# Kernel optimization log

Hardware: AMD Instinct MI355X
Metric: run time of the kernel (lower is better)

The kernel has to match this reference:

```python
import jax, jax.numpy as jnp
import numpy as np

N, E, G = 50000, 320000, 256
BN_EPS = 1e-5
HEADS = 4


def _bn(x, g, b):
    # eval-mode BatchNorm1d with running_mean=0, running_var=1
    return g * (x * np.float32(1.0 / np.sqrt(1.0 + BN_EPS))) + b


def _mlp(x, w1, b1, w2, b2):
    return jax.nn.relu(x @ w1 + b1) @ w2 + b2


def _gatv2(x, src, dst, ea, lw, lb, rw, rb, ew, att, bias):
    n = x.shape[0]
    H = HEADS
    C = lw.shape[1] // H
    # self-loops with edge_attr = mean of incoming edge features (fill_value='mean')
    deg = jax.ops.segment_sum(jnp.ones((ea.shape[0],), x.dtype), dst, num_segments=n)
    loop_ea = jax.ops.segment_sum(ea, dst, num_segments=n) / jnp.maximum(deg, 1.0)[:, None]
    ar = jnp.arange(n)
    s = jnp.concatenate([src, ar])
    d = jnp.concatenate([dst, ar])
    ea_all = jnp.concatenate([ea, loop_ea], axis=0)
    xl = (x @ lw + lb).reshape(n, H, C)   # lin_l (source / message features)
    xr = (x @ rw + rb).reshape(n, H, C)   # lin_r (target)
    ee = (ea_all @ ew).reshape(-1, H, C)  # lin_edge (no bias)
    m = jax.nn.leaky_relu(xl[s] + xr[d] + ee, 0.2)       # [E+N, H, C]
    a = jnp.einsum('ehc,hc->eh', m, att)                 # attention logits
    amax = jax.ops.segment_max(a, d, num_segments=n)
    ex = jnp.exp(a - amax[d])
    den = jax.ops.segment_sum(ex, d, num_segments=n)
    w = ex / den[d]                                      # scatter-softmax over target
    out = jax.ops.segment_sum(xl[s] * w[..., None], d, num_segments=n)
    return out.reshape(n, H * C) + bias


def _meta(x, ea, u, src, dst, batch, ep, gp, up):
    # EdgeModel -> NodeModel(GATv2 + relu) -> GlobalModel (residuals=False, eval dropout)
    ea2 = _mlp(jnp.concatenate([x[src], x[dst], ea], axis=1), *ep)
    xn = jax.nn.relu(_gatv2(x, src, dst, ea2, *gp))
    pooled = jax.ops.segment_sum(xn, batch, num_segments=G)
    u2 = _mlp(jnp.concatenate([u, pooled], axis=1), *up)
    return xn, ea2, u2


def _forward(x, edge_attr, e1_w1, e1_b1, e1_w2, e1_b2, g1_lw, g1_lb, g1_rw, g1_rb, g1_ew, g1_att, g1_bias, u1_w1, u1_b1, u1_w2, u1_b2, bn_n_g, bn_n_b, bn_e_g, bn_e_b, bn_u_g, bn_u_b, e2_w1, e2_b1, e2_w2, e2_b2, g2_lw, g2_lb, g2_rw, g2_rb, g2_ew, g2_att, g2_bias, u2_w1, u2_b1, u2_w2, u2_b2, fc1_w, fc1_b, fc2_w, fc2_b, src, dst, batch):
    u0 = jnp.zeros((G, 256), x.dtype)
    x1, ea1, u1 = _meta(x, edge_attr, u0, src, dst, batch,
                        (e1_w1, e1_b1, e1_w2, e1_b2),
                        (g1_lw, g1_lb, g1_rw, g1_rb, g1_ew, g1_att, g1_bias),
                        (u1_w1, u1_b1, u1_w2, u1_b2))
    x1 = _bn(x1, bn_n_g, bn_n_b)
    ea1 = _bn(ea1, bn_e_g, bn_e_b)
    u1 = _bn(u1, bn_u_g, bn_u_b)
    _, _, u2 = _meta(x1, ea1, u1, src, dst, batch,
                     (e2_w1, e2_b1, e2_w2, e2_b2),
                     (g2_lw, g2_lb, g2_rw, g2_rb, g2_ew, g2_att, g2_bias),
                     (u2_w1, u2_b1, u2_w2, u2_b2))
    h = jax.nn.relu(u2 @ fc1_w + fc1_b)
    return h @ fc2_w + fc2_b


def setup_inputs() -> dict:
    key = jax.random.key(0)
    ks = iter(jax.random.split(key, 64))
    rp = lambda shape: jax.random.normal(next(ks), shape, jnp.float32) * 0.05
    inp = {}
    inp['x'] = jax.random.normal(next(ks), (N, 64), jnp.float32)
    inp['edge_attr'] = jax.random.normal(next(ks), (E, 16), jnp.float32)
    # layer 1: EdgeModel(64,16,h=64,out=128), GATv2(64->256,H=4,edge=128), Global(256+256->256)
    inp.update(e1_w1=rp((144, 64)), e1_b1=rp((64,)), e1_w2=rp((64, 128)), e1_b2=rp((128,)))
    inp.update(g1_lw=rp((64, 256)), g1_lb=rp((256,)), g1_rw=rp((64, 256)), g1_rb=rp((256,)),
               g1_ew=rp((128, 256)), g1_att=rp((4, 64)), g1_bias=rp((256,)))
    inp.update(u1_w1=rp((512, 256)), u1_b1=rp((256,)), u1_w2=rp((256, 256)), u1_b2=rp((256,)))
    inp.update(bn_n_g=jnp.ones((256,), jnp.float32), bn_n_b=jnp.zeros((256,), jnp.float32),
               bn_e_g=jnp.ones((128,), jnp.float32), bn_e_b=jnp.zeros((128,), jnp.float32),
               bn_u_g=jnp.ones((256,), jnp.float32), bn_u_b=jnp.zeros((256,), jnp.float32))
    # layer 2: EdgeModel(256,128,h=128,out=128), GATv2(256->256,H=4,edge=128), Global
    inp.update(e2_w1=rp((640, 128)), e2_b1=rp((128,)), e2_w2=rp((128, 128)), e2_b2=rp((128,)))
    inp.update(g2_lw=rp((256, 256)), g2_lb=rp((256,)), g2_rw=rp((256, 256)), g2_rb=rp((256,)),
               g2_ew=rp((128, 256)), g2_att=rp((4, 64)), g2_bias=rp((256,)))
    inp.update(u2_w1=rp((512, 256)), u2_b1=rp((256,)), u2_w2=rp((256, 256)), u2_b2=rp((256,)))
    inp.update(fc1_w=rp((256, 64)), fc1_b=rp((64,)), fc2_w=rp((64, 1)), fc2_b=rp((1,)))
    inp['edge_index'] = jax.random.randint(next(ks), (2, E), 0, N, jnp.int64)
    inp['batch'] = jnp.sort(jax.random.randint(next(ks), (N,), 0, G, jnp.int64))
    return inp


def reference(x, edge_attr, e1_w1, e1_b1, e1_w2, e1_b2, g1_lw, g1_lb, g1_rw, g1_rb, g1_ew, g1_att, g1_bias, u1_w1, u1_b1, u1_w2, u1_b2, bn_n_g, bn_n_b, bn_e_g, bn_e_b, bn_u_g, bn_u_b, e2_w1, e2_b1, e2_w2, e2_b2, g2_lw, g2_lb, g2_rw, g2_rb, g2_ew, g2_att, g2_bias, u2_w1, u2_b1, u2_w2, u2_b2, fc1_w, fc1_b, fc2_w, fc2_b, edge_index, batch):
    return _forward(x, edge_attr, e1_w1, e1_b1, e1_w2, e1_b2, g1_lw, g1_lb, g1_rw, g1_rb, g1_ew, g1_att, g1_bias, u1_w1, u1_b1, u1_w2, u1_b2, bn_n_g, bn_n_b, bn_e_g, bn_e_b, bn_u_g, bn_u_b, e2_w1, e2_b1, e2_w2, e2_b2, g2_lw, g2_lb, g2_rw, g2_rb, g2_ew, g2_att, g2_bias, u2_w1, u2_b1, u2_w2, u2_b2, fc1_w, fc1_b, fc2_w, fc2_b, edge_index[0], edge_index[1], batch)
```

## Files before the change

kernel.cpp:

```cpp
#include <hip/hip_runtime.h>
#include <hip/hip_bf16.h>
#include <hip/hip_fp8.h>
#include <cstdint>
#include <cstddef>

#define INVS 0.99999500003749968f
#define G_GRAPHS 256

using bf16 = __hip_bfloat16;
using short8 = __attribute__((ext_vector_type(8))) short;
using floatx4 = __attribute__((ext_vector_type(4))) float;

__device__ __forceinline__ unsigned short f2bf(float v) {
    union { float f; unsigned u; } x; x.f = v;
    unsigned r = x.u + 0x7fffu + ((x.u >> 16) & 1u);
    return (unsigned short)(r >> 16);
}
__device__ __forceinline__ float bfu(unsigned short u) { return __uint_as_float((unsigned)u << 16); }
__device__ __forceinline__ unsigned char f2fp8(float v) {
    __hip_fp8_e4m3 q(v); return q.__x;
}
__device__ __forceinline__ float fp82f(unsigned char b) {
    __hip_fp8_e4m3 q; q.__x = b; return (float)q;
}

__global__ void degi_k(const int* __restrict__ dst, int* __restrict__ degi, int E) {
    int gid = blockIdx.x * 256 + threadIdx.x;
    if (gid < E) atomicAdd(&degi[dst[gid]], 1);
}

__global__ __launch_bounds__(1024) void scan_blk_k(const int* __restrict__ degi,
                                                   int* __restrict__ off,
                                                   int* __restrict__ bsum, int N) {
    __shared__ int buf[1024];
    int t = threadIdx.x;
    int base = blockIdx.x * 2048;
    int i0 = base + 2 * t, i1 = base + 2 * t + 1;
    int v0 = (i0 < N) ? (degi[i0] + 1) : 0;
    int v1 = (i1 < N) ? (degi[i1] + 1) : 0;
    int s = v0 + v1;
    buf[t] = s;
    __syncthreads();
    for (int ofs = 1; ofs < 1024; ofs <<= 1) {
        int add = (t >= ofs) ? buf[t - ofs] : 0;
        __syncthreads();
        buf[t] += add;
        __syncthreads();
    }
    int excl = buf[t] - s;
    if (i0 < N) off[i0] = excl;
    if (i1 < N) off[i1] = excl + v0;
    if (t == 1023) bsum[blockIdx.x] = buf[1023];
}

__global__ void scan_top_k(const int* __restrict__ bsum, int* __restrict__ boff,
                           int* __restrict__ off, int NBLK, int N) {
    if (threadIdx.x == 0 && blockIdx.x == 0) {
        int run = 0;
        for (int i = 0; i < NBLK; ++i) { boff[i] = run; run += bsum[i]; }
        off[N] = run;
    }
}

__global__ void scan_add_k(int* __restrict__ off, const int* __restrict__ boff, int N) {
    int gid = blockIdx.x * 256 + threadIdx.x;
    if (gid < N) off[gid] += boff[gid >> 11];
}

__global__ void fill_csr_k(const int* __restrict__ src, const int* __restrict__ dst,
                           const int* __restrict__ off, int* __restrict__ fillc,
                           int* __restrict__ csr_src, int* __restrict__ csr_dst,
                           int* __restrict__ csr_eid, int* __restrict__ slot_of,
                           int E, int N) {
    int gid = blockIdx.x * 256 + threadIdx.x;
    if (gid < E) {
        int d = dst[gid];
        int slot = off[d] + atomicAdd(&fillc[d], 1);
        csr_src[slot] = src[gid];
        csr_dst[slot] = d;
        csr_eid[slot] = gid;
        slot_of[gid] = slot;
    }
    if (gid < N) {
        int slot = off[gid + 1] - 1;
        csr_src[slot] = gid;
        csr_dst[slot] = gid;
        csr_eid[slot] = E + gid;
    }
}

__global__ void conv_weights1_k(const float* __restrict__ w1, const float* __restrict__ w2,
                                short* __restrict__ w1s, short* __restrict__ w2s) {
    int gid = blockIdx.x * 256 + threadIdx.x;
    if (gid < 1280) {
        int f = gid >> 6, lane = gid & 63;
        int kk = f >> 2, tt = f & 3;
        int n = tt * 16 + (lane & 15);
        int k0 = kk * 32 + (lane >> 4) * 8;
        short8 v;
        for (int j = 0; j < 8; ++j) {
            int k = k0 + j;
            v[j] = (k < 144) ? (short)f2bf(w1[k * 64 + n]) : (short)0;
        }
        *(short8*)(w1s + (long long)gid * 8) = v;
    } else if (gid < 2304) {
        int g2 = gid - 1280;
        int f = g2 >> 6, lane = g2 & 63;
        int kk = f >> 3, tt = f & 7;
        int n = tt * 16 + (lane & 15);
        int k0 = kk * 32 + (lane >> 4) * 8;
        short8 v;
        for (int j = 0; j < 8; ++j) v[j] = (short)f2bf(w2[(k0 + j) * 128 + n]);
        *(short8*)(w2s + (long long)g2 * 8) = v;
    }
}

__global__ void conv_ew_k(const float* __restrict__ ew, short* __restrict__ ews) {
    int gid = blockIdx.x * 256 + threadIdx.x;
    if (gid >= 4096) return;
    int f = gid >> 6, lane = gid & 63;
    int kk = f >> 4, tt = f & 15;
    int n = tt * 16 + (lane & 15);
    int k0 = kk * 32 + (lane >> 4) * 8;
    short8 v;
    for (int j = 0; j < 8; ++j) v[j] = (short)f2bf(ew[(k0 + j) * 256 + n]);
    *(short8*)(ews + (long long)gid * 8) = v;
}

template <int K>
__global__ void conv_nodew_k(const float* __restrict__ wl, const float* __restrict__ wr,
                             short* __restrict__ out) {
    int gid = blockIdx.x * 256 + threadIdx.x;
    if (gid >= (K / 32) * 32 * 64) return;
    int f = gid >> 6, lane = gid & 63;
    int kk = f >> 5, tt = f & 31;
    int n = tt * 16 + (lane & 15);
    int k0 = kk * 32 + (lane >> 4) * 8;
    short8 v;
    for (int j = 0; j < 8; ++j) {
        int k = k0 + j;
        float x = (n < 256) ? wl[k * 256 + n] : wr[k * 256 + (n - 256)];
        v[j] = (short)f2bf(x);
    }
    *(short8*)(out + (long long)gid * 8) = v;
}

__global__ void conv_pre2w_k(const float* __restrict__ w1, short* __restrict__ out) {
    int gid = blockIdx.x * 256 + threadIdx.x;
    if (gid >= 8 * 16 * 64) return;
    int f = gid >> 6, lane = gid & 63;
    int kk = f >> 4, tt = f & 15;
    int n = tt * 16 + (lane & 15);
    int k0 = kk * 32 + (lane >> 4) * 8;
    short8 v;
    for (int j = 0; j < 8; ++j) {
        int k = k0 + j;
        float x = (n < 128) ? w1[k * 128 + n] : w1[(256 + k) * 128 + (n - 128)];
        v[j] = (short)f2bf(x);
    }
    *(short8*)(out + (long long)gid * 8) = v;
}

__global__ __launch_bounds__(256) void edge_mlp1_mfma_k(
    const float* __restrict__ x, const float* __restrict__ ea,
    const int* __restrict__ src, const int* __restrict__ dst,
    const int* __restrict__ slot_of,
    const short* __restrict__ w1s, const float* __restrict__ b1,
    const short* __restrict__ w2s, const float* __restrict__ b2,
    bf16* __restrict__ out, int E) {
    __shared__ short At[32][168];
    __shared__ short Ht[32][72];
    __shared__ int sdv[32][2];
    __shared__ int slt[32];
    int t = threadIdx.x;
    long long e0 = (long long)blockIdx.x * 32;
    if (t < 64) {
        int r = t & 31;
        long long e = e0 + r;
        int v = 0;
        if (e < E) v = (t < 32) ? src[e] : dst[e];
        sdv[r][t >> 5] = v;
    } else if (t < 96) {
        int r = t - 64;
        long long e = e0 + r;
        slt[r] = (e < E) ? slot_of[e] : -1;
    }
    __syncthreads();
    for (int i = t; i < 32 * 40; i += 256) {
        int r = i / 40, c = i - r * 40;
        long long e = e0 + r;
        float4 v = {0.f, 0.f, 0.f, 0.f};
        if (e < E) {
            if (c < 16)      v = *(const float4*)(x + (long long)sdv[r][0] * 64 + c * 4);
            else if (c < 32) v = *(const float4*)(x + (long long)sdv[r][1] * 64 + (c - 16) * 4);
            else if (c < 36) v = *(const float4*)(ea + e * 16 + (c - 32) * 4);
        }
        ushort4 pk;
        pk.x = f2bf(v.x); pk.y = f2bf(v.y); pk.z = f2bf(v.z); pk.w = f2bf(v.w);
        *(ushort4*)&At[r][c * 4] = pk;
    }
    __syncthreads();

    int w = t >> 6, lane = t & 63;
    int m0 = (w & 1) * 16;
    int lr = lane & 15, lq = lane >> 4;

    int nq1 = (w >> 1) * 2;
    floatx4 acc[2];
    for (int i = 0; i < 2; ++i) acc[i] = (floatx4){0.f, 0.f, 0.f, 0.f};
    for (int kk = 0; kk < 5; ++kk) {
        short8 a = *(const short8*)&At[m0 + lr][kk * 32 + lq * 8];
        for (int tt = 0; tt < 2; ++tt) {
            short8 b = *(const short8*)(w1s + ((long long)((kk * 4 + nq1 + tt) * 64 + lane)) * 8);
            acc[tt] = __builtin_amdgcn_mfma_f32_16x16x32_bf16(a, b, acc[tt], 0, 0, 0);
        }
    }
    for (int tt = 0; tt < 2; ++tt) {
        int col = (nq1 + tt) * 16 + lr;
        float bv = b1[col];
        for (int r = 0; r < 4; ++r)
            Ht[m0 + lq * 4 + r][col] = (short)f2bf(fmaxf(acc[tt][r] + bv, 0.f));
    }
    __syncthreads();

    int nq2 = (w >> 1) * 4;
    floatx4 acc2[4];
    for (int i = 0; i < 4; ++i) acc2[i] = (floatx4){0.f, 0.f, 0.f, 0.f};
    for (int kk = 0; kk < 2; ++kk) {
        short8 a = *(const short8*)&Ht[m0 + lr][kk * 32 + lq * 8];
        for (int tt = 0; tt < 4; ++tt) {
            short8 b = *(const short8*)(w2s + ((long long)((kk * 8 + nq2 + tt) * 64 + lane)) * 8);
            acc2[tt] = __builtin_amdgcn_mfma_f32_16x16x32_bf16(a, b, acc2[tt], 0, 0, 0);
        }
    }
    for (int tt = 0; tt < 4; ++tt) {
        int col = (nq2 + tt) * 16 + lr;
        float bv = b2[col];
        for (int r = 0; r < 4; ++r)
            At[m0 + lq * 4 + r][col] = (short)f2bf(acc2[tt][r] + bv);
    }
    __syncthreads();
    for (int i = t; i < 512; i += 256) {
        int r = i >> 4, c = i & 15;
        int s = slt[r];
        if (s >= 0)
            *(short8*)(void*)(out + (long long)s * 128 + c * 8) = *(const short8*)&At[r][c * 8];
    }
}

template <int K, typename T>
__global__ __launch_bounds__(256) void node_linear_mfma_k(
    const T* x, const short* __restrict__ ws,
    const float* __restrict__ bl, const float* __restrict__ br,
    bf16* __restrict__ xl, bf16* xr, int N) {
    __shared__ short At[16][K + 8];
    __shared__ short Ot[16][520];
    int t = threadIdx.x;
    long long n0 = (long long)blockIdx.x * 16;
    if (sizeof(T) == 4) {
        for (int i = t; i < 16 * (K / 4); i += 256) {
            int r = i / (K / 4), c = i % (K / 4);
            long long n = n0 + r;
            float4 v = {0.f, 0.f, 0.f, 0.f};
            if (n < N) v = *(const float4*)((const float*)x + n * K + c * 4);
            ushort4 pk;
            pk.x = f2bf(v.x); pk.y = f2bf(v.y); pk.z = f2bf(v.z); pk.w = f2bf(v.w);
            *(ushort4*)&At[r][c * 4] = pk;
        }
    } else {
        for (int i = t; i < 16 * (K / 8); i += 256) {
            int r = i / (K / 8), c = i % (K / 8);
            long long n = n0 + r;
            short8 v = {0, 0, 0, 0, 0, 0, 0, 0};
            if (n < N) v = *(const short8*)(const void*)((const bf16*)x + n * K + c * 8);
            *(short8*)&At[r][c * 8] = v;
        }
    }
    __syncthreads();

    int w = t >> 6, lane = t & 63;
    int nq = w * 8;
    int lr = lane & 15, lq = lane >> 4;

    floatx4 acc[8];
    for (int i = 0; i < 8; ++i) acc[i] = (floatx4){0.f, 0.f, 0.f, 0.f};
    for (int kk = 0; kk < K / 32; ++kk) {
        short8 a = *(const short8*)&At[lr][kk * 32 + lq * 8];
        for (int tt = 0; tt < 8; ++tt) {
            short8 b = *(const short8*)(ws + ((long long)((kk * 32 + nq + tt) * 64 + lane)) * 8);
            acc[tt] = __builtin_amdgcn_mfma_f32_16x16x32_bf16(a, b, acc[tt], 0, 0, 0);
        }
    }
    for (int tt = 0; tt < 8; ++tt) {
        int col = (nq + tt) * 16 + lr;
        float bv = (col < 256) ? bl[col] : br[col - 256];
        for (int r = 0; r < 4; ++r)
            Ot[lq * 4 + r][col] = (short)f2bf(acc[tt][r] + bv);
    }
    __syncthreads();
    for (int i = t; i < 1024; i += 256) {
        int r = i >> 6, c = i & 63;
        long long n = n0 + r;
        if (n < N) {
            short8 v = *(const short8*)&Ot[r][c * 8];
            if (c < 32) *(short8*)(void*)(xl + n * 256 + c * 8) = v;
            else        *(short8*)(void*)(xr + n * 256 + (c - 32) * 8) = v;
        }
    }
}

__global__ __launch_bounds__(256) void pre_mfma_k(
    const bf16* __restrict__ x, const short* __restrict__ ws,
    const float* __restrict__ bx, bf16* __restrict__ out, int N) {
    __shared__ short At[16][264];
    __shared__ short Ot[16][264];
    int t = threadIdx.x;
    long long n0 = (long long)blockIdx.x * 16;
    for (int i = t; i < 512; i += 256) {
        int r = i >> 5, c = i & 31;
        long long n = n0 + r;
        short8 v = {0, 0, 0, 0, 0, 0, 0, 0};
        if (n < N) v = *(const short8*)(const void*)(x + n * 256 + c * 8);
        *(short8*)&At[r][c * 8] = v;
    }
    __syncthreads();

    int w = t >> 6, lane = t & 63;
    int nq = w * 4;
    int lr = lane & 15, lq = lane >> 4;

    floatx4 acc[4];
    for (int i = 0; i < 4; ++i) acc[i] = (floatx4){0.f, 0.f, 0.f, 0.f};
    for (int kk = 0; kk < 8; ++kk) {
        short8 a = *(const short8*)&At[lr][kk * 32 + lq * 8];
        for (int tt = 0; tt < 4; ++tt) {
            short8 b = *(const short8*)(ws + ((long long)((kk * 16 + nq + tt) * 64 + lane)) * 8);
            acc[tt] = __builtin_amdgcn_mfma_f32_16x16x32_bf16(a, b, acc[tt], 0, 0, 0);
        }
    }
    for (int tt = 0; tt < 4; ++tt) {
        int col = (nq + tt) * 16 + lr;
        float bv = bx[col];
        for (int r = 0; r < 4; ++r)
            Ot[lq * 4 + r][col] = (short)f2bf(acc[tt][r] + bv);
    }
    __syncthreads();
    for (int i = t; i < 512; i += 256) {
        int r = i >> 5, c = i & 31;
        long long n = n0 + r;
        if (n < N)
            *(short8*)(void*)(out + n * 256 + c * 8) = *(const short8*)&Ot[r][c * 8];
    }
}

__global__ __launch_bounds__(256) void gemm_ee_k(
    const bf16* __restrict__ ea_slot, const short* __restrict__ ews,
    unsigned char* __restrict__ ee8, int NT) {
    __shared__ short At[32][136];
    __shared__ unsigned char Et[32][264];
    int t = threadIdx.x;
    long long s0 = (long long)blockIdx.x * 32;
    for (int i = t; i < 32 * 16; i += 256) {
        int r = i >> 4, c = i & 15;
        long long s = s0 + r;
        short8 v = {0, 0, 0, 0, 0, 0, 0, 0};
        if (s < NT) v = *(const short8*)(const void*)(ea_slot + s * 128 + c * 8);
        *(short8*)&At[r][c * 8] = v;
    }
    __syncthreads();

    int w = t >> 6, lane = t & 63;
    int m0 = (w & 1) * 16, nq = (w >> 1) * 8;
    int lr = lane & 15, lq = lane >> 4;

    floatx4 acc[8];
    for (int i = 0; i < 8; ++i) acc[i] = (floatx4){0.f, 0.f, 0.f, 0.f};
    for (int kk = 0; kk < 4; ++kk) {
        short8 a = *(const short8*)&At[m0 + lr][kk * 32 + lq * 8];
        for (int tt = 0; tt < 8; ++tt) {
            short8 b = *(const short8*)(ews + ((long long)((kk * 16 + nq + tt) * 64 + lane)) * 8);
            acc[tt] = __builtin_amdgcn_mfma_f32_16x16x32_bf16(a, b, acc[tt], 0, 0, 0);
        }
    }
    for (int tt = 0; tt < 8; ++tt) {
        int col = (nq + tt) * 16 + lr;
        for (int r = 0; r < 4; ++r)
            Et[m0 + lq * 4 + r][col] = f2fp8(acc[tt][r]);
    }
    __syncthreads();
    for (int i = t; i < 2048; i += 256) {
        int r = i >> 6, c = i & 63;
        long long s = s0 + r;
        if (s < NT)
            *(unsigned*)(ee8 + s * 256 + c * 4) = *(const unsigned*)&Et[r][c * 4];
    }
}

__global__ __launch_bounds__(256) void loop_ee_k(unsigned char* __restrict__ ee8,
                                                 const int* __restrict__ off, int N) {
    int t = threadIdx.x;
    int w = t >> 6, lane = t & 63;
    int n = blockIdx.x * 4 + w;
    if (n >= N) return;
    int beg = off[n], end = off[n + 1] - 1;
    float a0 = 0.f, a1 = 0.f, a2 = 0.f, a3 = 0.f;
    for (int i = beg; i < end; ++i) {
        unsigned pk = *(const unsigned*)(ee8 + (long long)i * 256 + lane * 4);
        a0 += fp82f(pk & 0xff);
        a1 += fp82f((pk >> 8) & 0xff);
        a2 += fp82f((pk >> 16) & 0xff);
        a3 += fp82f(pk >> 24);
    }
    float dv = fmaxf((float)(end - beg), 1.f);
    unsigned o = (unsigned)f2fp8(a0 / dv)
               | ((unsigned)f2fp8(a1 / dv) << 8)
               | ((unsigned)f2fp8(a2 / dv) << 16)
               | ((unsigned)f2fp8(a3 / dv) << 24);
    *(unsigned*)(ee8 + (long long)end * 256 + lane * 4) = o;
}

template <bool L1>
__global__ __launch_bounds__(256) void gat_fused_k(
    const unsigned char* __restrict__ ee8, const bf16* __restrict__ xl, const bf16* xr,
    const int* __restrict__ off, const int* __restrict__ csr_src,
    const float* __restrict__ att, const float* __restrict__ bias,
    const float* __restrict__ bng, const float* __restrict__ bnb,
    const int* __restrict__ batch,
    bf16* x1bn, float* __restrict__ pooled, int N) {
    __shared__ float ps[4][260];
    __shared__ int bid[4];
    int t = threadIdx.x;
    int w = t >> 6, lane = t & 63;
    int n = blockIdx.x * 4 + w;
    bool valid = n < N;
    int c0 = lane * 4;
    float o0 = 0.f, o1 = 0.f, o2 = 0.f, o3 = 0.f;
    if (valid) {
        ushort4 xrp = *(const ushort4*)(const void*)(xr + (long long)n * 256 + c0);
        float xr0 = bfu(xrp.x), xr1 = bfu(xrp.y), xr2 = bfu(xrp.z), xr3 = bfu(xrp.w);
        float4 atv = *(const float4*)(att + c0);
        float a0 = 0.f, a1 = 0.f, a2 = 0.f, a3 = 0.f, dacc = 0.f;
        int beg = off[n], end = off[n + 1];
        ushort4 xlp;
        unsigned ep;
        {
            int sid = csr_src[beg];
            xlp = *(const ushort4*)(const void*)(xl + (long long)sid * 256 + c0);
            ep = *(const unsigned*)(ee8 + (long long)beg * 256 + c0);
        }
        for (int i = beg; i < end; ++i) {
            ushort4 cx = xlp;
            unsigned ce = ep;
            if (i + 1 < end) {
                int sid = csr_src[i + 1];
                xlp = *(const ushort4*)(const void*)(xl + (long long)sid * 256 + c0);
                ep = *(const unsigned*)(ee8 + (long long)(i + 1) * 256 + c0);
            }
            float x0 = bfu(cx.x), x1 = bfu(cx.y), x2 = bfu(cx.z), x3 = bfu(cx.w);
            float m0 = x0 + xr0 + fp82f(ce & 0xff);
            float m1 = x1 + xr1 + fp82f((ce >> 8) & 0xff);
            float m2 = x2 + xr2 + fp82f((ce >> 16) & 0xff);
            float m3 = x3 + xr3 + fp82f(ce >> 24);
            m0 = m0 > 0.f ? m0 : 0.2f * m0;
            m1 = m1 > 0.f ? m1 : 0.2f * m1;
            m2 = m2 > 0.f ? m2 : 0.2f * m2;
            m3 = m3 > 0.f ? m3 : 0.2f * m3;
            float p = atv.x * m0 + atv.y * m1 + atv.z * m2 + atv.w * m3;
            p += __shfl_xor(p, 1, 64);
            p += __shfl_xor(p, 2, 64);
            p += __shfl_xor(p, 4, 64);
            p += __shfl_xor(p, 8, 64);
            float ex = expf(p);
            a0 += ex * x0; a1 += ex * x1; a2 += ex * x2; a3 += ex * x3;
            dacc += ex;
        }
        float inv = 1.f / dacc;
        o0 = fmaxf(a0 * inv + bias[c0],     0.f);
        o1 = fmaxf(a1 * inv + bias[c0 + 1], 0.f);
        o2 = fmaxf(a2 * inv + bias[c0 + 2], 0.f);
        o3 = fmaxf(a3 * inv + bias[c0 + 3], 0.f);
        if (L1) {
            ushort4 o;
            o.x = f2bf(bng[c0]     * (o0 * INVS) + bnb[c0]);
            o.y = f2bf(bng[c0 + 1] * (o1 * INVS) + bnb[c0 + 1]);
            o.z = f2bf(bng[c0 + 2] * (o2 * INVS) + bnb[c0 + 2]);
            o.w = f2bf(bng[c0 + 3] * (o3 * INVS) + bnb[c0 + 3]);
            *(ushort4*)(void*)(x1bn + (long long)n * 256 + c0) = o;
        }
    }
    if (lane == 0) bid[w] = valid ? batch[n] : -1;
    ps[w][c0]     = o0;
    ps[w][c0 + 1] = o1;
    ps[w][c0 + 2] = o2;
    ps[w][c0 + 3] = o3;
    __syncthreads();
    int b0 = bid[0];
    bool same = (b0 >= 0)
             && (bid[1] < 0 || bid[1] == b0)
             && (bid[2] < 0 || bid[2] == b0)
             && (bid[3] < 0 || bid[3] == b0);
    if (same) {
        float s = ps[0][t] + ps[1][t] + ps[2][t] + ps[3][t];
        atomicAdd(&pooled[(long long)b0 * 256 + t], s);
    } else if (valid) {
        long long pb = (long long)bid[w] * 256 + c0;
        atomicAdd(&pooled[pb],     o0);
        atomicAdd(&pooled[pb + 1], o1);
        atomicAdd(&pooled[pb + 2], o2);
        atomicAdd(&pooled[pb + 3], o3);
    }
}

__global__ void global_mlp1_k(const float* __restrict__ pooled,
                              const float* __restrict__ w1, const float* __restrict__ b1,
                              const float* __restrict__ w2, const float* __restrict__ b2,
                              const float* __restrict__ bng, const float* __restrict__ bnb,
                              float* __restrict__ u1bn) {
    __shared__ float pr[256];
    __shared__ float h[256];
    int t = threadIdx.x, g = blockIdx.x;
    pr[t] = pooled[g * 256 + t];
    __syncthreads();
    float acc = b1[t];
    for (int k = 0; k < 256; ++k) acc += pr[k] * w1[(256 + k) * 256 + t];
    h[t] = fmaxf(acc, 0.f);
    __syncthreads();
    float a2 = b2[t];
    for (int k = 0; k < 256; ++k) a2 += h[k] * w2[k * 256 + t];
    u1bn[g * 256 + t] = bng[t] * (a2 * INVS) + bnb[t];
}

__global__ void conv_weights_k(const float* __restrict__ w1, const float* __restrict__ w2,
                               const float* __restrict__ b1,
                               const float* __restrict__ bg, const float* __restrict__ bb,
                               short* __restrict__ w1s, short* __restrict__ w2s,
                               float* __restrict__ b1x) {
    int gid = blockIdx.x * 256 + threadIdx.x;
    if (gid < 10240) {
        int f = gid >> 6, lane = gid & 63;
        int kk = f >> 3, tt = f & 7;
        int n = tt * 16 + (lane & 15);
        int k0 = kk * 32 + (lane >> 4) * 8;
        short8 v;
        for (int j = 0; j < 8; ++j) {
            int k = k0 + j;
            float x = w1[k * 128 + n];
            if (k >= 512) x *= bg[k - 512] * INVS;
            v[j] = (short)f2bf(x);
        }
        *(short8*)(w1s + (long long)gid * 8) = v;
    } else if (gid < 12288) {
        int g2 = gid - 10240;
        int f = g2 >> 6, lane = g2 & 63;
        int kk = f >> 3, tt = f & 7;
        int n = tt * 16 + (lane & 15);
        int k0 = kk * 32 + (lane >> 4) * 8;
        short8 v;
        for (int j = 0; j < 8; ++j) v[j] = (short)f2bf(w2[(k0 + j) * 128 + n]);
        *(short8*)(w2s + (long long)g2 * 8) = v;
    } else if (gid < 12544) {
        int j = gid - 12288;
        b1x[j] = 0.f;
    } else if (gid < 12672) {
        int j = gid - 12544;
        float acc = b1[j];
        for (int c = 0; c < 128; ++c) acc += bb[c] * w1[(512 + c) * 128 + j];
        b1x[128 + j] = acc;
    }
}

__global__ __launch_bounds__(256) void edge_mlp2_mfma_k(
    const bf16* __restrict__ xpre, bf16* __restrict__ ea_slot,
    const int* __restrict__ csr_src, const int* __restrict__ csr_dst,
    const int* __restrict__ csr_eid,
    const short* __restrict__ w1s,
    const short* __restrict__ w2s, const float* __restrict__ b2,
    int NT, int E) {
    __shared__ float Ps[32][132];
    __shared__ short At[32][136];
    __shared__ short Ht[32][136];
    __shared__ int sdv[32][3];
    int t = threadIdx.x;
    long long s0 = (long long)blockIdx.x * 32;
    if (t < 96) {
        int r = t & 31, which = t >> 5;
        long long s = s0 + r;
        int v = (which == 2) ? E : 0;
        if (s < NT) v = (which == 0) ? csr_src[s] : (which == 1 ? csr_dst[s] : csr_eid[s]);
        sdv[r][which] = v;
    }
    __syncthreads();
    for (int i = t; i < 512; i += 256) {
        int r = i >> 4, c = i & 15;
        long long s = s0 + r;
        bool ok = (s < NT) && (sdv[r][2] < E);
        float p[8];
        if (ok) {
            short8 vs = *(const short8*)(const void*)(xpre + (long long)sdv[r][0] * 256 + c * 8);
            short8 vd = *(const short8*)(const void*)(xpre + (long long)sdv[r][1] * 256 + 128 + c * 8);
            for (int j = 0; j < 8; ++j)
                p[j] = bfu((unsigned short)vs[j]) + bfu((unsigned short)vd[j]);
        } else {
            for (int j = 0; j < 8; ++j) p[j] = 0.f;
        }
        for (int j = 0; j < 8; ++j) Ps[r][c * 8 + j] = p[j];
    }
    for (int i = t; i < 512; i += 256) {
        int r = i >> 4, c = i & 15;
        long long s = s0 + r;
        short8 v = {0, 0, 0, 0, 0, 0, 0, 0};
        if (s < NT && sdv[r][2] < E)
            v = *(const short8*)(const void*)(ea_slot + s * 128 + c * 8);
        *(short8*)&At[r][c * 8] = v;
    }
    __syncthreads();

    int w = t >> 6, lane = t & 63;
    int m0 = (w & 1) * 16;
    int nq = (w >> 1) * 4;
    int lr = lane & 15, lq = lane >> 4;

    floatx4 acc[4];
    for (int tt = 0; tt < 4; ++tt) {
        int col = (nq + tt) * 16 + lr;
        for (int r = 0; r < 4; ++r) acc[tt][r] = Ps[m0 + lq * 4 + r][col];
    }
    for (int kk = 0; kk < 4; ++kk) {
        short8 a = *(const short8*)&At[m0 + lr][kk * 32 + lq * 8];
        for (int tt = 0; tt < 4; ++tt) {
            short8 b = *(const short8*)(w1s + ((long long)(((16 + kk) * 8 + nq + tt) * 64 + lane)) * 8);
            acc[tt] = __builtin_amdgcn_mfma_f32_16x16x32_bf16(a, b, acc[tt], 0, 0, 0);
        }
    }
    for (int tt = 0; tt < 4; ++tt) {
        int col = (nq + tt) * 16 + lr;
        for (int r = 0; r < 4; ++r)
            Ht[m0 + lq * 4 + r][col] = (short)f2bf(fmaxf(acc[tt][r], 0.f));
    }
    __syncthreads();

    floatx4 acc2[4];
    for (int i = 0; i < 4; ++i) acc2[i] = (floatx4){0.f, 0.f, 0.f, 0.f};
    for (int kk = 0; kk < 4; ++kk) {
        short8 a = *(const short8*)&Ht[m0 + lr][kk * 32 + lq * 8];
        for (int tt = 0; tt < 4; ++tt) {
            short8 b = *(const short8*)(w2s + ((long long)((kk * 8 + nq + tt) * 64 + lane)) * 8);
            acc2[tt] = __builtin_amdgcn_mfma_f32_16x16x32_bf16(a, b, acc2[tt], 0, 0, 0);
        }
    }
    for (int tt = 0; tt < 4; ++tt) {
        int col = (nq + tt) * 16 + lr;
        float bv = b2[col];
        for (int r = 0; r < 4; ++r)
            At[m0 + lq * 4 + r][col] = (short)f2bf(acc2[tt][r] + bv);
    }
    __syncthreads();
    for (int i = t; i < 512; i += 256) {
        int r = i >> 4, c = i & 15;
        long long s = s0 + r;
        if (s < NT && sdv[r][2] < E)
            *(short8*)(void*)(ea_slot + s * 128 + c * 8) = *(const short8*)&At[r][c * 8];
    }
}

__global__ void final_mlp_k(const float* __restrict__ u1bn, const float* __restrict__ pooled,
                            const float* __restrict__ w1, const float* __restrict__ b1,
                            const float* __restrict__ w2, const float* __restrict__ b2,
                            const float* __restrict__ f1w, const float* __restrict__ f1b,
                            const float* __restrict__ f2w, const float* __restrict__ f2b,
                            float* __restrict__ out) {
    __shared__ float ub[256], pb[256], h[256], u2[256];
    int t = threadIdx.x, g = blockIdx.x;
    ub[t] = u1bn[g * 256 + t];
    pb[t] = pooled[g * 256 + t];
    __syncthreads();
    float acc = b1[t];
    for (int k = 0; k < 256; ++k)
        acc += ub[k] * w1[k * 256 + t] + pb[k] * w1[(256 + k) * 256 + t];
    h[t] = fmaxf(acc, 0.f);
    __syncthreads();
    float a2 = b2[t];
    for (int k = 0; k < 256; ++k) a2 += h[k] * w2[k * 256 + t];
    u2[t] = a2;
    __syncthreads();
    float fv = 0.f;
    if (t < 64) {
        float a3 = f1b[t];
        for (int k = 0; k < 256; ++k) a3 += u2[k] * f1w[k * 64 + t];
        fv = fmaxf(a3, 0.f) * f2w[t];
    }
    for (int off = 32; off; off >>= 1) fv += __shfl_down(fv, off, 64);
    if (t == 0) out[g] = fv + f2b[0];
}

extern "C" void kernel_launch(void* const* d_in, const int* in_sizes, int n_in,
                              void* d_out, int out_size, void* d_ws, size_t ws_size,
                              hipStream_t stream) {
    const float* x         = (const float*)d_in[0];
    const float* edge_attr = (const float*)d_in[1];
    const float* e1_w1 = (const float*)d_in[2];
    const float* e1_b1 = (const float*)d_in[3];
    const float* e1_w2 = (const float*)d_in[4];
    const float* e1_b2 = (const float*)d_in[5];
    const float* g1_lw = (const float*)d_in[6];
    const float* g1_lb = (const float*)d_in[7];
    const float* g1_rw = (const float*)d_in[8];
    const float* g1_rb = (const float*)d_in[9];
    const float* g1_ew = (const float*)d_in[10];
    const float* g1_att = (const float*)d_in[11];
    const float* g1_bias = (const float*)d_in[12];
    const float* u1_w1 = (const float*)d_in[13];
    const float* u1_b1 = (const float*)d_in[14];
    const float* u1_w2 = (const float*)d_in[15];
    const float* u1_b2 = (const float*)d_in[16];
    const float* bn_n_g = (const float*)d_in[17];
    const float* bn_n_b = (const float*)d_in[18];
    const float* bn_e_g = (const float*)d_in[19];
    const float* bn_e_b = (const float*)d_in[20];
    const float* bn_u_g = (const float*)d_in[21];
    const float* bn_u_b = (const float*)d_in[22];
    const float* e2_w1 = (const float*)d_in[23];
    const float* e2_b1 = (const float*)d_in[24];
    const float* e2_w2 = (const float*)d_in[25];
    const float* e2_b2 = (const float*)d_in[26];
    const float* g2_lw = (const float*)d_in[27];
    const float* g2_lb = (const float*)d_in[28];
    const float* g2_rw = (const float*)d_in[29];
    const float* g2_rb = (const float*)d_in[30];
    const float* g2_ew = (const float*)d_in[31];
    const float* g2_att = (const float*)d_in[32];
    const float* g2_bias = (const float*)d_in[33];
    const float* u2_w1 = (const float*)d_in[34];
    const float* u2_b1 = (const float*)d_in[35];
    const float* u2_w2 = (const float*)d_in[36];
    const float* u2_b2 = (const float*)d_in[37];
    const float* fc1_w = (const float*)d_in[38];
    const float* fc1_b = (const float*)d_in[39];
    const float* fc2_w = (const float*)d_in[40];
    const float* fc2_b = (const float*)d_in[41];
    const int* edge_index = (const int*)d_in[42];
    const int* batch = (const int*)d_in[43];

    const int N = in_sizes[0] / 64;
    const int E = in_sizes[1] / 16;
    const int NT = E + N;
    const int G = G_GRAPHS;
    const int* src = edge_index;
    const int* dst = edge_index + E;
    const int NB = (NT + 31) / 32;
    const int NSB = (N + 2047) / 2048;

    char* p = (char*)d_ws;
    auto alloc = [&](size_t bytes) { char* r = p; p += (bytes + 255) & ~(size_t)255; return r; };
    bf16* eabuf = (bf16*)alloc((size_t)NT * 128 * 2);
    bf16* xl    = (bf16*)alloc((size_t)N * 256 * 2);
    bf16* xr    = (bf16*)alloc((size_t)N * 256 * 2);
    bf16* x1bn  = xr;
    unsigned char* ee8 = (unsigned char*)alloc((size_t)NT * 256);
    int* degi   = (int*)alloc((size_t)N * 4);
    int* off    = (int*)alloc((size_t)(N + 1) * 4);
    int* fillc  = (int*)alloc((size_t)N * 4);
    int* csr_src = (int*)alloc((size_t)NT * 4);
    int* csr_dst = (int*)alloc((size_t)NT * 4);
    int* csr_eid = (int*)alloc((size_t)NT * 4);
    int* slot_of = (int*)alloc((size_t)E * 4);
    int* bsum   = (int*)alloc((size_t)(NSB + 1) * 4);
    int* boff   = (int*)alloc((size_t)(NSB + 1) * 4);
    float* pooled = (float*)alloc((size_t)G * 256 * 4);
    float* u1bn = (float*)alloc((size_t)G * 256 * 4);
    short* w1s  = (short*)alloc((size_t)20 * 8 * 64 * 8 * 2);
    short* w2s  = (short*)alloc((size_t)4 * 8 * 64 * 8 * 2);
    float* b1x  = (float*)alloc((size_t)256 * 4);
    short* w1s1 = (short*)alloc((size_t)5 * 4 * 64 * 8 * 2);
    short* w2s1 = (short*)alloc((size_t)2 * 8 * 64 * 8 * 2);
    short* ews1 = (short*)alloc((size_t)4 * 16 * 64 * 8 * 2);
    short* ews2 = (short*)alloc((size_t)4 * 16 * 64 * 8 * 2);
    short* nw1  = (short*)alloc((size_t)2 * 32 * 64 * 8 * 2);
    short* nw2  = (short*)alloc((size_t)8 * 32 * 64 * 8 * 2);
    short* nwp  = (short*)alloc((size_t)8 * 16 * 64 * 8 * 2);

    hipMemsetAsync(degi, 0, (size_t)N * 4, stream);
    hipMemsetAsync(fillc, 0, (size_t)N * 4, stream);
    hipMemsetAsync(pooled, 0, (size_t)G * 256 * 4, stream);
    degi_k<<<(E + 255) / 256, 256, 0, stream>>>(dst, degi, E);
    scan_blk_k<<<NSB, 1024, 0, stream>>>(degi, off, bsum, N);
    scan_top_k<<<1, 64, 0, stream>>>(bsum, boff, off, NSB, N);
    scan_add_k<<<(N + 255) / 256, 256, 0, stream>>>(off, boff, N);
    fill_csr_k<<<(max(E, N) + 255) / 256, 256, 0, stream>>>(src, dst, off, fillc,
                                                            csr_src, csr_dst, csr_eid,
                                                            slot_of, E, N);

    conv_weights1_k<<<9, 256, 0, stream>>>(e1_w1, e1_w2, w1s1, w2s1);
    conv_ew_k<<<16, 256, 0, stream>>>(g1_ew, ews1);
    conv_ew_k<<<16, 256, 0, stream>>>(g2_ew, ews2);
    conv_nodew_k<64><<<16, 256, 0, stream>>>(g1_lw, g1_rw, nw1);
    conv_nodew_k<256><<<64, 256, 0, stream>>>(g2_lw, g2_rw, nw2);
    conv_pre2w_k<<<32, 256, 0, stream>>>(e2_w1, nwp);
    edge_mlp1_mfma_k<<<(E + 31) / 32, 256, 0, stream>>>(x, edge_attr, src, dst, slot_of,
                                                        w1s1, e1_b1, w2s1, e1_b2, eabuf, E);
    node_linear_mfma_k<64, float><<<(N + 15) / 16, 256, 0, stream>>>(x, nw1, g1_lb, g1_rb, xl, xr, N);
    gemm_ee_k<<<NB, 256, 0, stream>>>(eabuf, ews1, ee8, NT);
    loop_ee_k<<<(N + 3) / 4, 256, 0, stream>>>(ee8, off, N);
    gat_fused_k<true><<<(N + 3) / 4, 256, 0, stream>>>(ee8, xl, xr, off, csr_src,
                                                       g1_att, g1_bias, bn_n_g, bn_n_b,
                                                       batch, x1bn, pooled, N);
    global_mlp1_k<<<G, 256, 0, stream>>>(pooled, u1_w1, u1_b1, u1_w2, u1_b2, bn_u_g, bn_u_b, u1bn);

    conv_weights_k<<<50, 256, 0, stream>>>(e2_w1, e2_w2, e2_b1, bn_e_g, bn_e_b, w1s, w2s, b1x);
    pre_mfma_k<<<(N + 15) / 16, 256, 0, stream>>>(x1bn, nwp, b1x, xl, N);
    edge_mlp2_mfma_k<<<NB, 256, 0, stream>>>(xl, eabuf, csr_src, csr_dst, csr_eid,
                                             w1s, w2s, e2_b2, NT, E);
    node_linear_mfma_k<256, bf16><<<(N + 15) / 16, 256, 0, stream>>>(x1bn, nw2, g2_lb, g2_rb, xl, xr, N);
    hipMemsetAsync(pooled, 0, (size_t)G * 256 * 4, stream);
    gemm_ee_k<<<NB, 256, 0, stream>>>(eabuf, ews2, ee8, NT);
    loop_ee_k<<<(N + 3) / 4, 256, 0, stream>>>(ee8, off, N);
    gat_fused_k<false><<<(N + 3) / 4, 256, 0, stream>>>(ee8, xl, xr, off, csr_src,
                                                        g2_att, g2_bias, nullptr, nullptr,
                                                        batch, nullptr, pooled, N);
    final_mlp_k<<<G, 256, 0, stream>>>(u1bn, pooled, u2_w1, u2_b1, u2_w2, u2_b2,
                                       fc1_w, fc1_b, fc2_w, fc2_b, (float*)d_out);
}
```

Measured before the change: 859.7 us.

## Fuse edge-feature projection into edge MLPs and compute self-loop term inside GAT

The lin_edge GEMM that produced fp8 edge embeddings now runs in the epilogue of both edge-MLP kernels, working on the MLP output already held in shared memory. This removes the separate gemm_ee pass and its re-read of the bf16 edge buffer. The self-loop mean edge feature is now accumulated during the GAT aggregation loop, so the loop_ee kernel and its extra pass over ee8 are gone. In exchange the edge-MLP kernels do more work per block and use more registers and LDS, which could lower occupancy. The self-loop mean is now taken over the fp8-decoded per-edge values, which is the same input the removed loop_ee kernel used.

```diff
diff --git a/kernel.cpp b/kernel.cpp
--- a/kernel.cpp
+++ b/kernel.cpp
@@ -167,9 +167,11 @@
     const int* __restrict__ slot_of,
     const short* __restrict__ w1s, const float* __restrict__ b1,
     const short* __restrict__ w2s, const float* __restrict__ b2,
-    bf16* __restrict__ out, int E) {
+    const short* __restrict__ ews,
+    bf16* __restrict__ out, unsigned char* __restrict__ ee8, int E) {
     __shared__ short At[32][168];
     __shared__ short Ht[32][72];
+    __shared__ unsigned char Et[32][272];
     __shared__ int sdv[32][2];
     __shared__ int slt[32];
     int t = threadIdx.x;
@@ -240,11 +242,35 @@
             At[m0 + lq * 4 + r][col] = (short)f2bf(acc2[tt][r] + bv);
     }
     __syncthreads();
+    {
+        int nq3 = (w >> 1) * 8;
+        floatx4 acc3[8];
+        for (int i = 0; i < 8; ++i) acc3[i] = (floatx4){0.f, 0.f, 0.f, 0.f};
+        for (int kk = 0; kk < 4; ++kk) {
+            short8 a = *(const short8*)&At[m0 + lr][kk * 32 + lq * 8];
+            for (int tt = 0; tt < 8; ++tt) {
+                short8 b = *(const short8*)(ews + ((long long)((kk * 16 + nq3 + tt) * 64 + lane)) * 8);
+                acc3[tt] = __builtin_amdgcn_mfma_f32_16x16x32_bf16(a, b, acc3[tt], 0, 0, 0);
+            }
+        }
+        for (int tt = 0; tt < 8; ++tt) {
+            int col = (nq3 + tt) * 16 + lr;
+            for (int r = 0; r < 4; ++r)
+                Et[m0 + lq * 4 + r][col] = f2fp8(acc3[tt][r]);
+        }
+    }
     for (int i = t; i < 512; i += 256) {
         int r = i >> 4, c = i & 15;
         int s = slt[r];
         if (s >= 0)
             *(short8*)(void*)(out + (long long)s * 128 + c * 8) = *(const short8*)&At[r][c * 8];
+    }
+    __syncthreads();
+    for (int i = t; i < 512; i += 256) {
+        int r = i >> 4, c = i & 15;
+        int s = slt[r];
+        if (s >= 0)
+            *(uint4*)(ee8 + (long long)s * 256 + c * 16) = *(const uint4*)&Et[r][c * 16];
     }
 }
 
@@ -353,72 +379,6 @@
     }
 }
 
-__global__ __launch_bounds__(256) void gemm_ee_k(
-    const bf16* __restrict__ ea_slot, const short* __restrict__ ews,
-    unsigned char* __restrict__ ee8, int NT) {
-    __shared__ short At[32][136];
-    __shared__ unsigned char Et[32][264];
-    int t = threadIdx.x;
-    long long s0 = (long long)blockIdx.x * 32;
-    for (int i = t; i < 32 * 16; i += 256) {
-        int r = i >> 4, c = i & 15;
-        long long s = s0 + r;
-        short8 v = {0, 0, 0, 0, 0, 0, 0, 0};
-        if (s < NT) v = *(const short8*)(const void*)(ea_slot + s * 128 + c * 8);
-        *(short8*)&At[r][c * 8] = v;
-    }
-    __syncthreads();
-
-    int w = t >> 6, lane = t & 63;
-    int m0 = (w & 1) * 16, nq = (w >> 1) * 8;
-    int lr = lane & 15, lq = lane >> 4;
-
-    floatx4 acc[8];
-    for (int i = 0; i < 8; ++i) acc[i] = (floatx4){0.f, 0.f, 0.f, 0.f};
-    for (int kk = 0; kk < 4; ++kk) {
-        short8 a = *(const short8*)&At[m0 + lr][kk * 32 + lq * 8];
-        for (int tt = 0; tt < 8; ++tt) {
-            short8 b = *(const short8*)(ews + ((long long)((kk * 16 + nq + tt) * 64 + lane)) * 8);
-            acc[tt] = __builtin_amdgcn_mfma_f32_16x16x32_bf16(a, b, acc[tt], 0, 0, 0);
-        }
-    }
-    for (int tt = 0; tt < 8; ++tt) {
-        int col = (nq + tt) * 16 + lr;
-        for (int r = 0; r < 4; ++r)
-            Et[m0 + lq * 4 + r][col] = f2fp8(acc[tt][r]);
-    }
-    __syncthreads();
-    for (int i = t; i < 2048; i += 256) {
-        int r = i >> 6, c = i & 63;
-        long long s = s0 + r;
-        if (s < NT)
-            *(unsigned*)(ee8 + s * 256 + c * 4) = *(const unsigned*)&Et[r][c * 4];
-    }
-}
-
-__global__ __launch_bounds__(256) void loop_ee_k(unsigned char* __restrict__ ee8,
-                                                 const int* __restrict__ off, int N) {
-    int t = threadIdx.x;
-    int w = t >> 6, lane = t & 63;
-    int n = blockIdx.x * 4 + w;
-    if (n >= N) return;
-    int beg = off[n], end = off[n + 1] - 1;
-    float a0 = 0.f, a1 = 0.f, a2 = 0.f, a3 = 0.f;
-    for (int i = beg; i < end; ++i) {
-        unsigned pk = *(const unsigned*)(ee8 + (long long)i * 256 + lane * 4);
-        a0 += fp82f(pk & 0xff);
-        a1 += fp82f((pk >> 8) & 0xff);
-        a2 += fp82f((pk >> 16) & 0xff);
-        a3 += fp82f(pk >> 24);
-    }
-    float dv = fmaxf((float)(end - beg), 1.f);
-    unsigned o = (unsigned)f2fp8(a0 / dv)
-               | ((unsigned)f2fp8(a1 / dv) << 8)
-               | ((unsigned)f2fp8(a2 / dv) << 16)
-               | ((unsigned)f2fp8(a3 / dv) << 24);
-    *(unsigned*)(ee8 + (long long)end * 256 + lane * 4) = o;
-}
-
 template <bool L1>
 __global__ __launch_bounds__(256) void gat_fused_k(
     const unsigned char* __restrict__ ee8, const bf16* __restrict__ xl, const bf16* xr,
@@ -437,10 +397,12 @@
     float o0 = 0.f, o1 = 0.f, o2 = 0.f, o3 = 0.f;
     if (valid) {
         ushort4 xrp = *(const ushort4*)(const void*)(xr + (long long)n * 256 + c0);
+        ushort4 xop = *(const ushort4*)(const void*)(xl + (long long)n * 256 + c0);
         float xr0 = bfu(xrp.x), xr1 = bfu(xrp.y), xr2 = bfu(xrp.z), xr3 = bfu(xrp.w);
         float4 atv = *(const float4*)(att + c0);
         float a0 = 0.f, a1 = 0.f, a2 = 0.f, a3 = 0.f, dacc = 0.f;
-        int beg = off[n], end = off[n + 1];
+        float es0 = 0.f, es1 = 0.f, es2 = 0.f, es3 = 0.f;
+        int beg = off[n], end1 = off[n + 1] - 1;
         ushort4 xlp;
         unsigned ep;
         {
@@ -448,19 +410,44 @@
             xlp = *(const ushort4*)(const void*)(xl + (long long)sid * 256 + c0);
             ep = *(const unsigned*)(ee8 + (long long)beg * 256 + c0);
         }
-        for (int i = beg; i < end; ++i) {
+        for (int i = beg; i < end1; ++i) {
             ushort4 cx = xlp;
             unsigned ce = ep;
-            if (i + 1 < end) {
+            if (i + 1 < end1) {
                 int sid = csr_src[i + 1];
                 xlp = *(const ushort4*)(const void*)(xl + (long long)sid * 256 + c0);
                 ep = *(const unsigned*)(ee8 + (long long)(i + 1) * 256 + c0);
             }
             float x0 = bfu(cx.x), x1 = bfu(cx.y), x2 = bfu(cx.z), x3 = bfu(cx.w);
-            float m0 = x0 + xr0 + fp82f(ce & 0xff);
-            float m1 = x1 + xr1 + fp82f((ce >> 8) & 0xff);
-            float m2 = x2 + xr2 + fp82f((ce >> 16) & 0xff);
-            float m3 = x3 + xr3 + fp82f(ce >> 24);
+            float e0 = fp82f(ce & 0xff);
+            float e1 = fp82f((ce >> 8) & 0xff);
+            float e2 = fp82f((ce >> 16) & 0xff);
+            float e3 = fp82f(ce >> 24);
+            es0 += e0; es1 += e1; es2 += e2; es3 += e3;
+            float m0 = x0 + xr0 + e0;
+            float m1 = x1 + xr1 + e1;
+            float m2 = x2 + xr2 + e2;
+            float m3 = x3 + xr3 + e3;
+            m0 = m0 > 0.f ? m0 : 0.2f * m0;
+            m1 = m1 > 0.f ? m1 : 0.2f * m1;
+            m2 = m2 > 0.f ? m2 : 0.2f * m2;
+            m3 = m3 > 0.f ? m3 : 0.2f * m3;
+            float p = atv.x * m0 + atv.y * m1 + atv.z * m2 + atv.w * m3;
+            p += __shfl_xor(p, 1, 64);
+            p += __shfl_xor(p, 2, 64);
+            p += __shfl_xor(p, 4, 64);
+            p += __shfl_xor(p, 8, 64);
+            float ex = expf(p);
+            a0 += ex * x0; a1 += ex * x1; a2 += ex * x2; a3 += ex * x3;
+            dacc += ex;
+        }
+        {
+            float rdv = 1.f / fmaxf((float)(end1 - beg), 1.f);
+            float x0 = bfu(xop.x), x1 = bfu(xop.y), x2 = bfu(xop.z), x3 = bfu(xop.w);
+            float m0 = x0 + xr0 + es0 * rdv;
+            float m1 = x1 + xr1 + es1 * rdv;
+            float m2 = x2 + xr2 + es2 * rdv;
+            float m3 = x3 + xr3 + es3 * rdv;
             m0 = m0 > 0.f ? m0 : 0.2f * m0;
             m1 = m1 > 0.f ? m1 : 0.2f * m1;
             m2 = m2 > 0.f ? m2 : 0.2f * m2;
@@ -570,16 +557,18 @@
 }
 
 __global__ __launch_bounds__(256) void edge_mlp2_mfma_k(
-    const bf16* __restrict__ xpre, bf16* __restrict__ ea_slot,
+    const bf16* __restrict__ xpre, const bf16* __restrict__ ea_slot,
     const int* __restrict__ csr_src, const int* __restrict__ csr_dst,
     const int* __restrict__ csr_eid,
     const short* __restrict__ w1s,
     const short* __restrict__ w2s, const float* __restrict__ b2,
-    int NT, int E) {
+    const short* __restrict__ ews,
+    unsigned char* __restrict__ ee8, int NT, int E) {
     __shared__ float Ps[32][132];
     __shared__ short At[32][136];
     __shared__ short Ht[32][136];
     __shared__ int sdv[32][3];
+    unsigned char* Et = (unsigned char*)&Ps[0][0];
     int t = threadIdx.x;
     long long s0 = (long long)blockIdx.x * 32;
     if (t < 96) {
@@ -655,11 +644,29 @@
             At[m0 + lq * 4 + r][col] = (short)f2bf(acc2[tt][r] + bv);
     }
     __syncthreads();
+    {
+        int nq3 = (w >> 1) * 8;
+        floatx4 acc3[8];
+        for (int i = 0; i < 8; ++i) acc3[i] = (floatx4){0.f, 0.f, 0.f, 0.f};
+        for (int kk = 0; kk < 4; ++kk) {
+            short8 a = *(const short8*)&At[m0 + lr][kk * 32 + lq * 8];
+            for (int tt = 0; tt < 8; ++tt) {
+                short8 b = *(const short8*)(ews + ((long long)((kk * 16 + nq3 + tt) * 64 + lane)) * 8);
+                acc3[tt] = __builtin_amdgcn_mfma_f32_16x16x32_bf16(a, b, acc3[tt], 0, 0, 0);
+            }
+        }
+        for (int tt = 0; tt < 8; ++tt) {
+            int col = (nq3 + tt) * 16 + lr;
+            for (int r = 0; r < 4; ++r)
+                Et[(m0 + lq * 4 + r) * 272 + col] = f2fp8(acc3[tt][r]);
+        }
+    }
+    __syncthreads();
     for (int i = t; i < 512; i += 256) {
         int r = i >> 4, c = i & 15;
         long long s = s0 + r;
         if (s < NT && sdv[r][2] < E)
-            *(short8*)(void*)(ea_slot + s * 128 + c * 8) = *(const short8*)&At[r][c * 8];
+            *(uint4*)(ee8 + s * 256 + c * 16) = *(const uint4*)(Et + r * 272 + c * 16);
     }
 }
 
@@ -797,10 +804,9 @@
     conv_nodew_k<256><<<64, 256, 0, stream>>>(g2_lw, g2_rw, nw2);
     conv_pre2w_k<<<32, 256, 0, stream>>>(e2_w1, nwp);
     edge_mlp1_mfma_k<<<(E + 31) / 32, 256, 0, stream>>>(x, edge_attr, src, dst, slot_of,
-                                                        w1s1, e1_b1, w2s1, e1_b2, eabuf, E);
+                                                        w1s1, e1_b1, w2s1, e1_b2, ews1,
+                                                        eabuf, ee8, E);
     node_linear_mfma_k<64, float><<<(N + 15) / 16, 256, 0, stream>>>(x, nw1, g1_lb, g1_rb, xl, xr, N);
-    gemm_ee_k<<<NB, 256, 0, stream>>>(eabuf, ews1, ee8, NT);
-    loop_ee_k<<<(N + 3) / 4, 256, 0, stream>>>(ee8, off, N);
     gat_fused_k<true><<<(N + 3) / 4, 256, 0, stream>>>(ee8, xl, xr, off, csr_src,
                                                        g1_att, g1_bias, bn_n_g, bn_n_b,
                                                        batch, x1bn, pooled, N);
@@ -809,11 +815,9 @@
     conv_weights_k<<<50, 256, 0, stream>>>(e2_w1, e2_w2, e2_b1, bn_e_g, bn_e_b, w1s, w2s, b1x);
     pre_mfma_k<<<(N + 15) / 16, 256, 0, stream>>>(x1bn, nwp, b1x, xl, N);
     edge_mlp2_mfma_k<<<NB, 256, 0, stream>>>(xl, eabuf, csr_src, csr_dst, csr_eid,
-                                             w1s, w2s, e2_b2, NT, E);
+                                             w1s, w2s, e2_b2, ews2, ee8, NT, E);
     node_linear_mfma_k<256, bf16><<<(N + 15) / 16, 256, 0, stream>>>(x1bn, nw2, g2_lb, g2_rb, xl, xr, N);
     hipMemsetAsync(pooled, 0, (size_t)G * 256 * 4, stream);
-    gemm_ee_k<<<NB, 256, 0, stream>>>(eabuf, ews2, ee8, NT);
-    loop_ee_k<<<(N + 3) / 4, 256, 0, stream>>>(ee8, off, N);
     gat_fused_k<false><<<(N + 3) / 4, 256, 0, stream>>>(ee8, xl, xr, off, csr_src,
                                                         g2_att, g2_bias, nullptr, nullptr,
                                                         batch, nullptr, pooled, N);
```

After: 847.5 us. Within noise of the previous version (-1.4%).
